# Kernel optimization log

Measured on AMD Instinct MI355X. Metric: run time of the kernel, lower is better.

Reference implementation:

```python
import jax, jax.numpy as jnp
import numpy as np

NUM_HEADS = 12


def setup_inputs() -> dict:
    key = jax.random.key(0)
    ks = jax.random.split(key, 20)
    T, B, D = 1024, 8, 768
    s = 1.0 / np.sqrt(D)
    inp = {
        "query": jax.random.normal(ks[0], (T, B, D), jnp.float32),
        "key": jax.random.normal(ks[1], (T, B, D), jnp.float32),
        "value": jax.random.normal(ks[2], (T, B, D), jnp.float32),
        "ls_len": 512,
    }
    names = ["Wq", "Wk", "Wv", "Wqm", "Wkm", "Wvm", "Wo"]
    for i, n in enumerate(names):
        inp[n] = jax.random.normal(ks[3 + i], (D, D), jnp.float32) * s
        inp["b" + n[1:]] = jnp.zeros((D,), jnp.float32)
    return inp


def reference(query, key, value, ls_len, Wq, bq, Wk, bk, Wv, bv,
              Wqm, bqm, Wkm, bkm, Wvm, bvm, Wo, bo):
    T, B, D = query.shape
    H = NUM_HEADS
    hd = D // H
    scaling = float(hd) ** -0.5

    def proj(x, W, b):
        return x @ W.T + b

    # modal-split projections along the sequence (dim 0), then re-concat
    q = jnp.concatenate([proj(query[:ls_len], Wq, bq),
                         proj(query[ls_len:], Wqm, bqm)], axis=0) * scaling
    k = jnp.concatenate([proj(key[:ls_len], Wk, bk),
                         proj(key[ls_len:], Wkm, bkm)], axis=0)
    v = jnp.concatenate([proj(value[:ls_len], Wv, bv),
                         proj(value[ls_len:], Wvm, bvm)], axis=0)

    # (T, B, D) -> (B*H, T, hd)
    def to_heads(x):
        return x.reshape(x.shape[0], B * H, hd).transpose(1, 0, 2)

    q, k, v = to_heads(q), to_heads(k), to_heads(v)
    scores = jnp.einsum("bth,bsh->bts", q, k)        # (B*H, T, S)
    attn = jax.nn.softmax(scores, axis=-1)
    out = jnp.einsum("bts,bsh->bth", attn, v)        # (B*H, T, hd)
    out = out.transpose(1, 0, 2).reshape(T, B, D)
    return out @ Wo.T + bo
```

## Files before the change

### kernel.cpp

```cpp
#include <hip/hip_runtime.h>

#define T_  1024
#define B_  8
#define D_  768
#define H_  12
#define HD_ 64
#define BH_ 96
#define M_  8192
#define XSZ 6291456ull
#define WSZ 589824ull

typedef __attribute__((ext_vector_type(8))) short short8;
typedef __attribute__((ext_vector_type(4))) float f32x4;

__device__ __forceinline__ unsigned short f2bf(float f) {
    unsigned int u = __float_as_uint(f);
    u += 0x7FFF + ((u >> 16) & 1);
    return (unsigned short)(u >> 16);
}

__device__ __forceinline__ void g2lds16(const unsigned short* g, unsigned short* l) {
    __builtin_amdgcn_global_load_lds(
        (const __attribute__((address_space(1))) unsigned int*)(g),
        (__attribute__((address_space(3))) unsigned int*)(l),
        16, 0, 0);
}

__global__ __launch_bounds__(256)
void convert_kernel(const float* __restrict__ q, const float* __restrict__ k,
                    const float* __restrict__ v,
                    const float* __restrict__ wq, const float* __restrict__ wk,
                    const float* __restrict__ wv, const float* __restrict__ wqm,
                    const float* __restrict__ wkm, const float* __restrict__ wvm,
                    const float* __restrict__ wo,
                    unsigned short* __restrict__ dst)
{
    const int seg = blockIdx.y;
    const float* s; size_t off, n;
    switch (seg) {
        case 0: s = q;   off = 0;               n = XSZ; break;
        case 1: s = k;   off = XSZ;             n = XSZ; break;
        case 2: s = v;   off = 2*XSZ;           n = XSZ; break;
        case 3: s = wq;  off = 3*XSZ;           n = WSZ; break;
        case 4: s = wk;  off = 3*XSZ +   WSZ;   n = WSZ; break;
        case 5: s = wv;  off = 3*XSZ + 2*WSZ;   n = WSZ; break;
        case 6: s = wqm; off = 3*XSZ + 3*WSZ;   n = WSZ; break;
        case 7: s = wkm; off = 3*XSZ + 4*WSZ;   n = WSZ; break;
        case 8: s = wvm; off = 3*XSZ + 5*WSZ;   n = WSZ; break;
        default:s = wo;  off = 3*XSZ + 6*WSZ;   n = WSZ; break;
    }
    unsigned short* d = dst + off;
    const size_t stride = (size_t)gridDim.x * blockDim.x;
    for (size_t i = (size_t)blockIdx.x * blockDim.x + threadIdx.x; i < n / 4; i += stride) {
        const float4 f = reinterpret_cast<const float4*>(s)[i];
        ushort4 o;
        o.x = f2bf(f.x); o.y = f2bf(f.y); o.z = f2bf(f.z); o.w = f2bf(f.w);
        reinterpret_cast<ushort4*>(d)[i] = o;
    }
}

__device__ __forceinline__ void stage_tile64(const unsigned short* __restrict__ A,
                                             const unsigned short* __restrict__ B,
                                             int m0, int n0, int ks,
                                             unsigned short* lds, int buf, int tid)
{
    const int w = tid >> 6, l = tid & 63;
    const int rsub = l >> 3;
    const int csw  = (l & 7) ^ rsub;
    const int koff = ks * 64 + csw * 8;
    #pragma unroll
    for (int p = 0; p < 4; ++p) {
        const int rbase = p * 32 + w * 8;
        const int row   = rbase + rsub;
        g2lds16(&A[(size_t)(m0 + row) * D_ + koff],
                &lds[buf * 16384 + rbase * 64]);
        g2lds16(&B[(size_t)(n0 + row) * D_ + koff],
                &lds[buf * 16384 + 8192 + rbase * 64]);
    }
}

__device__ __forceinline__ void mfma_step64(const unsigned short* lds, int buf,
                                            int wr, int wc, int lr, int lg,
                                            f32x4 acc[4][4])
{
    #pragma unroll
    for (int kk = 0; kk < 2; ++kk) {
        short8 a[4], b[4];
        #pragma unroll
        for (int m = 0; m < 4; ++m) {
            const int row  = wr * 64 + 16 * m + lr;
            const int slot = (kk * 4 + lg) ^ (lr & 7);
            a[m] = *reinterpret_cast<const short8*>(
                &lds[buf * 16384 + row * 64 + slot * 8]);
        }
        #pragma unroll
        for (int n = 0; n < 4; ++n) {
            const int row  = wc * 64 + 16 * n + lr;
            const int slot = (kk * 4 + lg) ^ (lr & 7);
            b[n] = *reinterpret_cast<const short8*>(
                &lds[buf * 16384 + 8192 + row * 64 + slot * 8]);
        }
        #pragma unroll
        for (int m = 0; m < 4; ++m)
            #pragma unroll
            for (int n = 0; n < 4; ++n)
                acc[m][n] = __builtin_amdgcn_mfma_f32_16x16x32_bf16(a[m], b[n], acc[m][n], 0, 0, 0);
    }
}

#define GEMM_CORE(Aptr, Bptr)                                                  \
    f32x4 acc[4][4];                                                           \
    _Pragma("unroll") for (int m = 0; m < 4; ++m)                              \
        _Pragma("unroll") for (int n = 0; n < 4; ++n)                          \
            acc[m][n] = (f32x4){0.f, 0.f, 0.f, 0.f};                           \
    stage_tile64(Aptr, Bptr, m0, n0, 0, lds, 0, tid);                          \
    asm volatile("s_waitcnt vmcnt(0)" ::: "memory");                           \
    __builtin_amdgcn_s_barrier();                                              \
    for (int ks = 0; ks < 12; ++ks) {                                          \
        __builtin_amdgcn_sched_barrier(0);                                     \
        if (ks < 11) stage_tile64(Aptr, Bptr, m0, n0, ks + 1, lds, (ks + 1) & 1, tid); \
        mfma_step64(lds, ks & 1, wr, wc, lr, lg, acc);                         \
        asm volatile("s_waitcnt vmcnt(0) lgkmcnt(0)" ::: "memory");            \
        __builtin_amdgcn_sched_barrier(0);                                     \
        __builtin_amdgcn_s_barrier();                                          \
        __builtin_amdgcn_sched_barrier(0);                                     \
    }

__global__ __launch_bounds__(256)
void qkv_gemm(const unsigned short* __restrict__ xb,
              const unsigned short* __restrict__ wb,
              const int* __restrict__ ls_ptr,
              const float* __restrict__ bq,  const float* __restrict__ bk,
              const float* __restrict__ bv,  const float* __restrict__ bqm,
              const float* __restrict__ bkm, const float* __restrict__ bvm,
              unsigned short* __restrict__ qh, unsigned short* __restrict__ kh,
              unsigned short* __restrict__ vt)
{
    __shared__ unsigned short lds[32768];
    const int bid = blockIdx.x;
    const int L   = (bid & 7) * 144 + (bid >> 3);
    const int z   = L / 384;
    const int rem = L - z * 384;
    const int mi  = rem / 6;
    const int ni  = rem - mi * 6;
    const int m0 = mi * 128, n0 = ni * 128;

    const int tid = threadIdx.x;
    const int w = tid >> 6, l = tid & 63, lr = l & 15, lg = l >> 4;
    const int wr = w >> 1, wc = w & 1;

    const bool modal = (m0 >= ls_ptr[0] * B_);
    const unsigned short* A = xb + (size_t)z * XSZ;
    const unsigned short* W = wb + (size_t)(z + (modal ? 3 : 0)) * WSZ;
    const float* bias = modal ? (z == 0 ? bqm : z == 1 ? bkm : bvm)
                              : (z == 0 ? bq  : z == 1 ? bk  : bv);

    GEMM_CORE(A, W)

    float bn[4];
    #pragma unroll
    for (int n = 0; n < 4; ++n) bn[n] = bias[n0 + wc * 64 + 16 * n + lr];

    if (z < 2) {
        unsigned short* dst = (z == 0) ? qh : kh;
        const float scale = (z == 0) ? 0.18033688011112042f : 1.0f;
        #pragma unroll
        for (int m = 0; m < 4; ++m) {
            const int grb = m0 + wr * 64 + 16 * m + 4 * lg;
            #pragma unroll
            for (int n = 0; n < 4; ++n) {
                const int gc = n0 + wc * 64 + 16 * n + lr;
                const int h = gc >> 6, e = gc & 63;
                #pragma unroll
                for (int j = 0; j < 4; ++j) {
                    const int gr = grb + j, t = gr >> 3, b = gr & 7;
                    dst[((size_t)(b * H_ + h) * T_ + t) * HD_ + e] =
                        f2bf((acc[m][n][j] + bn[n]) * scale);
                }
            }
        }
    } else {
        #pragma unroll
        for (int m = 0; m < 4; ++m) {
            const int grb = m0 + wr * 64 + 16 * m + 4 * lg;
            #pragma unroll
            for (int n = 0; n < 4; ++n) {
                const int gc = n0 + wc * 64 + 16 * n + lr;
                const int h = gc >> 6, e = gc & 63;
                #pragma unroll
                for (int j = 0; j < 4; ++j) {
                    const int gr = grb + j, t = gr >> 3, b = gr & 7;
                    vt[((size_t)(b * H_ + h) * HD_ + e) * T_ + t] =
                        f2bf(acc[m][n][j] + bn[n]);
                }
            }
        }
    }
}

__global__ __launch_bounds__(256)
void out_gemm(const unsigned short* __restrict__ aob,
              const unsigned short* __restrict__ wo,
              const float* __restrict__ bo, float* __restrict__ out)
{
    __shared__ unsigned short lds[32768];
    const int bid = blockIdx.x;
    const int L   = (bid & 7) * 48 + (bid >> 3);
    const int mi  = L / 6, ni = L - mi * 6;
    const int m0 = mi * 128, n0 = ni * 128;

    const int tid = threadIdx.x;
    const int w = tid >> 6, l = tid & 63, lr = l & 15, lg = l >> 4;
    const int wr = w >> 1, wc = w & 1;

    GEMM_CORE(aob, wo)

    float bn[4];
    #pragma unroll
    for (int n = 0; n < 4; ++n) bn[n] = bo[n0 + wc * 64 + 16 * n + lr];

    #pragma unroll
    for (int m = 0; m < 4; ++m) {
        const int grb = m0 + wr * 64 + 16 * m + 4 * lg;
        #pragma unroll
        for (int n = 0; n < 4; ++n) {
            const int gc = n0 + wc * 64 + 16 * n + lr;
            #pragma unroll
            for (int j = 0; j < 4; ++j) {
                const int gr = grb + j;
                out[(size_t)gr * D_ + gc] = acc[m][n][j] + bn[n];
            }
        }
    }
}

__global__ __launch_bounds__(256)
void attn_kernel_bf16(const unsigned short* __restrict__ qh,
                      const unsigned short* __restrict__ kh,
                      const unsigned short* __restrict__ vt,
                      unsigned short* __restrict__ aob)
{
    const int bid = blockIdx.x;
    const int L   = (bid & 7) * 192 + (bid >> 3);
    const int bh  = L >> 4;
    const int qt  = L & 15;

    const int tid = threadIdx.x;
    const int w   = tid >> 6;
    const int l   = tid & 63;
    const int lr  = l & 15;
    const int lg  = l >> 4;

    __shared__ unsigned short Ks[64 * 64];
    __shared__ unsigned short Vt[64 * 64];
    __shared__ unsigned short Ps[64 * 64];

    const size_t qk_head = (size_t)bh * T_ * HD_;
    const size_t vt_head = (size_t)bh * HD_ * T_;

    short8 qf[2];
    #pragma unroll
    for (int c = 0; c < 2; ++c)
        qf[c] = *reinterpret_cast<const short8*>(
            &qh[qk_head + (size_t)(qt * 64 + 16 * w + lr) * HD_ + 8 * lg + 32 * c]);

    const short one_bf = (short)0x3F80;
    const short8 ones8 = {one_bf, one_bf, one_bf, one_bf,
                          one_bf, one_bf, one_bf, one_bf};

    f32x4 o[4];
    #pragma unroll
    for (int ef = 0; ef < 4; ++ef) o[ef] = (f32x4){0.f, 0.f, 0.f, 0.f};
    f32x4 lsumf = (f32x4){0.f, 0.f, 0.f, 0.f};

    for (int kt = 0; kt < 16; ++kt) {
        __syncthreads();
        #pragma unroll
        for (int p = 0; p < 2; ++p) {
            const int slot = tid + p * 256;
            const int row  = slot >> 3;
            const int ch   = slot & 7;
            const int sw   = (ch ^ (row & 7)) * 8;
            const short8 kd = *reinterpret_cast<const short8*>(
                &kh[qk_head + (size_t)(kt * 64 + row) * HD_ + 8 * ch]);
            *reinterpret_cast<short8*>(&Ks[row * 64 + sw]) = kd;
            const short8 vd = *reinterpret_cast<const short8*>(
                &vt[vt_head + (size_t)row * T_ + kt * 64 + 8 * ch]);
            *reinterpret_cast<short8*>(&Vt[row * 64 + sw]) = vd;
        }
        __syncthreads();

        f32x4 s[4];
        #pragma unroll
        for (int nf = 0; nf < 4; ++nf) s[nf] = (f32x4){0.f, 0.f, 0.f, 0.f};
        #pragma unroll
        for (int c = 0; c < 2; ++c) {
            #pragma unroll
            for (int nf = 0; nf < 4; ++nf) {
                const int row = 16 * nf + lr;
                const short8 kb = *reinterpret_cast<const short8*>(
                    &Ks[row * 64 + ((8 * lg + 32 * c) ^ ((row & 7) << 3))]);
                s[nf] = __builtin_amdgcn_mfma_f32_16x16x32_bf16(qf[c], kb, s[nf], 0, 0, 0);
            }
        }

        #pragma unroll
        for (int r = 0; r < 4; ++r) {
            const int q  = 16 * w + 4 * lg + r;
            const int qx = ((4 * lg + r) & 7) << 3;
            #pragma unroll
            for (int nf = 0; nf < 4; ++nf)
                Ps[q * 64 + ((16 * nf + lr) ^ qx)] =
                    f2bf(exp2f(s[nf][r] - 16.0f));
        }
        __syncthreads();

        const int prow = 16 * w + lr;
        #pragma unroll
        for (int c = 0; c < 2; ++c) {
            const short8 pa = *reinterpret_cast<const short8*>(
                &Ps[prow * 64 + ((8 * lg + 32 * c) ^ ((prow & 7) << 3))]);
            #pragma unroll
            for (int ef = 0; ef < 4; ++ef) {
                const int vrow = 16 * ef + lr;
                const short8 vb = *reinterpret_cast<const short8*>(
                    &Vt[vrow * 64 + ((8 * lg + 32 * c) ^ ((vrow & 7) << 3))]);
                o[ef] = __builtin_amdgcn_mfma_f32_16x16x32_bf16(pa, vb, o[ef], 0, 0, 0);
            }
            lsumf = __builtin_amdgcn_mfma_f32_16x16x32_bf16(pa, ones8, lsumf, 0, 0, 0);
        }
    }

    const int b = bh / H_, h = bh % H_;
    #pragma unroll
    for (int r = 0; r < 4; ++r) {
        const int t = qt * 64 + 16 * w + 4 * lg + r;
        const float inv = 1.0f / lsumf[r];
        #pragma unroll
        for (int ef = 0; ef < 4; ++ef)
            aob[((size_t)t * B_ + b) * D_ + h * HD_ + 16 * ef + lr] =
                f2bf(o[ef][r] * inv);
    }
}

extern "C" void kernel_launch(void* const* d_in, const int* in_sizes, int n_in,
                              void* d_out, int out_size, void* d_ws, size_t ws_size,
                              hipStream_t stream)
{
    const float* query = (const float*)d_in[0];
    const float* keyi  = (const float*)d_in[1];
    const float* value = (const float*)d_in[2];
    const int*   lsp   = (const int*)  d_in[3];
    const float* Wq  = (const float*)d_in[4],  *bq  = (const float*)d_in[5];
    const float* Wk  = (const float*)d_in[6],  *bk  = (const float*)d_in[7];
    const float* Wv  = (const float*)d_in[8],  *bv  = (const float*)d_in[9];
    const float* Wqm = (const float*)d_in[10], *bqm = (const float*)d_in[11];
    const float* Wkm = (const float*)d_in[12], *bkm = (const float*)d_in[13];
    const float* Wvm = (const float*)d_in[14], *bvm = (const float*)d_in[15];
    const float* Wo  = (const float*)d_in[16], *bo  = (const float*)d_in[17];

    unsigned short* ws = (unsigned short*)d_ws;
    unsigned short* xb  = ws;
    unsigned short* wb  = xb + 3 * XSZ;
    unsigned short* qh  = wb + 7 * WSZ;
    unsigned short* kh  = qh + XSZ;
    unsigned short* vt  = kh + XSZ;
    unsigned short* aob = vt + XSZ;

    dim3 gc_(512, 10);
    convert_kernel<<<gc_, 256, 0, stream>>>(query, keyi, value,
                                            Wq, Wk, Wv, Wqm, Wkm, Wvm, Wo, xb);

    qkv_gemm<<<1152, 256, 0, stream>>>(xb, wb, lsp, bq, bk, bv, bqm, bkm, bvm,
                                       qh, kh, vt);

    attn_kernel_bf16<<<1536, 256, 0, stream>>>(qh, kh, vt, aob);

    out_gemm<<<384, 256, 0, stream>>>(aob, wb + 6 * WSZ, bo, (float*)d_out);
}
```

Measured before the change: 197.1 us.

## Halve GEMM k-tile, double-buffer attention K/V with async LDS loads, 128-query blocks

The shared GEMM core now stages 32-wide k-slices instead of 64, which halves LDS per block and allows more resident blocks, at the cost of twice as many barriers. The attention kernel moves to 512-thread blocks covering 128 queries, so each K/V tile is reused by twice as many query rows. K/V tiles are now loaded with direct global-to-LDS loads into a double buffer, prefetching the next tile while the current one is computed. This replaces the old register-staged loads and the two syncthreads that had no overlap between loading and compute.

```diff
diff --git a/kernel.cpp b/kernel.cpp
--- a/kernel.cpp
+++ b/kernel.cpp
@@ -59,53 +59,45 @@
     }
 }
 
-__device__ __forceinline__ void stage_tile64(const unsigned short* __restrict__ A,
+__device__ __forceinline__ void stage_tile32(const unsigned short* __restrict__ A,
                                              const unsigned short* __restrict__ B,
                                              int m0, int n0, int ks,
                                              unsigned short* lds, int buf, int tid)
 {
     const int w = tid >> 6, l = tid & 63;
-    const int rsub = l >> 3;
-    const int csw  = (l & 7) ^ rsub;
-    const int koff = ks * 64 + csw * 8;
-    #pragma unroll
-    for (int p = 0; p < 4; ++p) {
-        const int rbase = p * 32 + w * 8;
+    const int rsub = l >> 2;
+    const int cg   = (l & 3) ^ ((l >> 3) & 3);
+    const int koff = ks * 32 + cg * 8;
+    #pragma unroll
+    for (int p = 0; p < 2; ++p) {
+        const int rbase = p * 64 + w * 16;
         const int row   = rbase + rsub;
         g2lds16(&A[(size_t)(m0 + row) * D_ + koff],
-                &lds[buf * 16384 + rbase * 64]);
+                &lds[buf * 8192 + rbase * 32]);
         g2lds16(&B[(size_t)(n0 + row) * D_ + koff],
-                &lds[buf * 16384 + 8192 + rbase * 64]);
-    }
-}
-
-__device__ __forceinline__ void mfma_step64(const unsigned short* lds, int buf,
+                &lds[buf * 8192 + 4096 + rbase * 32]);
+    }
+}
+
+__device__ __forceinline__ void mfma_step32(const unsigned short* lds, int buf,
                                             int wr, int wc, int lr, int lg,
                                             f32x4 acc[4][4])
 {
-    #pragma unroll
-    for (int kk = 0; kk < 2; ++kk) {
-        short8 a[4], b[4];
-        #pragma unroll
-        for (int m = 0; m < 4; ++m) {
-            const int row  = wr * 64 + 16 * m + lr;
-            const int slot = (kk * 4 + lg) ^ (lr & 7);
-            a[m] = *reinterpret_cast<const short8*>(
-                &lds[buf * 16384 + row * 64 + slot * 8]);
-        }
-        #pragma unroll
-        for (int n = 0; n < 4; ++n) {
-            const int row  = wc * 64 + 16 * n + lr;
-            const int slot = (kk * 4 + lg) ^ (lr & 7);
-            b[n] = *reinterpret_cast<const short8*>(
-                &lds[buf * 16384 + 8192 + row * 64 + slot * 8]);
-        }
-        #pragma unroll
-        for (int m = 0; m < 4; ++m)
-            #pragma unroll
-            for (int n = 0; n < 4; ++n)
-                acc[m][n] = __builtin_amdgcn_mfma_f32_16x16x32_bf16(a[m], b[n], acc[m][n], 0, 0, 0);
-    }
+    const int slot = (lg ^ ((lr >> 1) & 3)) * 8;
+    short8 a[4], b[4];
+    #pragma unroll
+    for (int m = 0; m < 4; ++m)
+        a[m] = *reinterpret_cast<const short8*>(
+            &lds[buf * 8192 + (wr * 64 + 16 * m + lr) * 32 + slot]);
+    #pragma unroll
+    for (int n = 0; n < 4; ++n)
+        b[n] = *reinterpret_cast<const short8*>(
+            &lds[buf * 8192 + 4096 + (wc * 64 + 16 * n + lr) * 32 + slot]);
+    #pragma unroll
+    for (int m = 0; m < 4; ++m)
+        #pragma unroll
+        for (int n = 0; n < 4; ++n)
+            acc[m][n] = __builtin_amdgcn_mfma_f32_16x16x32_bf16(a[m], b[n], acc[m][n], 0, 0, 0);
 }
 
 #define GEMM_CORE(Aptr, Bptr)                                                  \
@@ -113,13 +105,13 @@
     _Pragma("unroll") for (int m = 0; m < 4; ++m)                              \
         _Pragma("unroll") for (int n = 0; n < 4; ++n)                          \
             acc[m][n] = (f32x4){0.f, 0.f, 0.f, 0.f};                           \
-    stage_tile64(Aptr, Bptr, m0, n0, 0, lds, 0, tid);                          \
+    stage_tile32(Aptr, Bptr, m0, n0, 0, lds, 0, tid);                          \
     asm volatile("s_waitcnt vmcnt(0)" ::: "memory");                           \
     __builtin_amdgcn_s_barrier();                                              \
-    for (int ks = 0; ks < 12; ++ks) {                                          \
+    for (int ks = 0; ks < 24; ++ks) {                                          \
         __builtin_amdgcn_sched_barrier(0);                                     \
-        if (ks < 11) stage_tile64(Aptr, Bptr, m0, n0, ks + 1, lds, (ks + 1) & 1, tid); \
-        mfma_step64(lds, ks & 1, wr, wc, lr, lg, acc);                         \
+        if (ks < 23) stage_tile32(Aptr, Bptr, m0, n0, ks + 1, lds, (ks + 1) & 1, tid); \
+        mfma_step32(lds, ks & 1, wr, wc, lr, lg, acc);                         \
         asm volatile("s_waitcnt vmcnt(0) lgkmcnt(0)" ::: "memory");            \
         __builtin_amdgcn_sched_barrier(0);                                     \
         __builtin_amdgcn_s_barrier();                                          \
@@ -136,7 +128,7 @@
               unsigned short* __restrict__ qh, unsigned short* __restrict__ kh,
               unsigned short* __restrict__ vt)
 {
-    __shared__ unsigned short lds[32768];
+    __shared__ unsigned short lds[16384];
     const int bid = blockIdx.x;
     const int L   = (bid & 7) * 144 + (bid >> 3);
     const int z   = L / 384;
@@ -203,7 +195,7 @@
               const unsigned short* __restrict__ wo,
               const float* __restrict__ bo, float* __restrict__ out)
 {
-    __shared__ unsigned short lds[32768];
+    __shared__ unsigned short lds[16384];
     const int bid = blockIdx.x;
     const int L   = (bid & 7) * 48 + (bid >> 3);
     const int mi  = L / 6, ni = L - mi * 6;
@@ -234,16 +226,28 @@
     }
 }
 
-__global__ __launch_bounds__(256)
+__device__ __forceinline__ void stage_kv(const unsigned short* __restrict__ khh,
+                                         const unsigned short* __restrict__ vth,
+                                         int kt, unsigned short* KsB,
+                                         unsigned short* VtB, int w, int l)
+{
+    const int rbase = w * 8;
+    const int row   = rbase + (l >> 3);
+    const int cg    = (l & 7) ^ ((l >> 3) & 7);
+    g2lds16(&khh[(size_t)(kt * 64 + row) * HD_ + cg * 8], &KsB[rbase * 64]);
+    g2lds16(&vth[(size_t)row * T_ + kt * 64 + cg * 8],    &VtB[rbase * 64]);
+}
+
+__global__ __launch_bounds__(512)
 void attn_kernel_bf16(const unsigned short* __restrict__ qh,
                       const unsigned short* __restrict__ kh,
                       const unsigned short* __restrict__ vt,
                       unsigned short* __restrict__ aob)
 {
     const int bid = blockIdx.x;
-    const int L   = (bid & 7) * 192 + (bid >> 3);
-    const int bh  = L >> 4;
-    const int qt  = L & 15;
+    const int L   = (bid & 7) * 96 + (bid >> 3);
+    const int bh  = L >> 3;
+    const int qt  = L & 7;
 
     const int tid = threadIdx.x;
     const int w   = tid >> 6;
@@ -251,18 +255,19 @@
     const int lr  = l & 15;
     const int lg  = l >> 4;
 
-    __shared__ unsigned short Ks[64 * 64];
-    __shared__ unsigned short Vt[64 * 64];
-    __shared__ unsigned short Ps[64 * 64];
-
+    __shared__ unsigned short Ks[2][4096];
+    __shared__ unsigned short Vt[2][4096];
+    __shared__ unsigned short Ps[8192];
+
+    const unsigned short* khh = kh + (size_t)bh * T_ * HD_;
+    const unsigned short* vth = vt + (size_t)bh * HD_ * T_;
     const size_t qk_head = (size_t)bh * T_ * HD_;
-    const size_t vt_head = (size_t)bh * HD_ * T_;
 
     short8 qf[2];
     #pragma unroll
     for (int c = 0; c < 2; ++c)
         qf[c] = *reinterpret_cast<const short8*>(
-            &qh[qk_head + (size_t)(qt * 64 + 16 * w + lr) * HD_ + 8 * lg + 32 * c]);
+            &qh[qk_head + (size_t)(qt * 128 + 16 * w + lr) * HD_ + 8 * lg + 32 * c]);
 
     const short one_bf = (short)0x3F80;
     const short8 ones8 = {one_bf, one_bf, one_bf, one_bf,
@@ -273,22 +278,15 @@
     for (int ef = 0; ef < 4; ++ef) o[ef] = (f32x4){0.f, 0.f, 0.f, 0.f};
     f32x4 lsumf = (f32x4){0.f, 0.f, 0.f, 0.f};
 
+    stage_kv(khh, vth, 0, Ks[0], Vt[0], w, l);
+    asm volatile("s_waitcnt vmcnt(0)" ::: "memory");
+    __builtin_amdgcn_s_barrier();
+
+    int buf = 0;
     for (int kt = 0; kt < 16; ++kt) {
-        __syncthreads();
-        #pragma unroll
-        for (int p = 0; p < 2; ++p) {
-            const int slot = tid + p * 256;
-            const int row  = slot >> 3;
-            const int ch   = slot & 7;
-            const int sw   = (ch ^ (row & 7)) * 8;
-            const short8 kd = *reinterpret_cast<const short8*>(
-                &kh[qk_head + (size_t)(kt * 64 + row) * HD_ + 8 * ch]);
-            *reinterpret_cast<short8*>(&Ks[row * 64 + sw]) = kd;
-            const short8 vd = *reinterpret_cast<const short8*>(
-                &vt[vt_head + (size_t)row * T_ + kt * 64 + 8 * ch]);
-            *reinterpret_cast<short8*>(&Vt[row * 64 + sw]) = vd;
-        }
-        __syncthreads();
+        __builtin_amdgcn_sched_barrier(0);
+        if (kt < 15)
+            stage_kv(khh, vth, kt + 1, Ks[buf ^ 1], Vt[buf ^ 1], w, l);
 
         f32x4 s[4];
         #pragma unroll
@@ -297,9 +295,8 @@
         for (int c = 0; c < 2; ++c) {
             #pragma unroll
             for (int nf = 0; nf < 4; ++nf) {
-                const int row = 16 * nf + lr;
                 const short8 kb = *reinterpret_cast<const short8*>(
-                    &Ks[row * 64 + ((8 * lg + 32 * c) ^ ((row & 7) << 3))]);
+                    &Ks[buf][(16 * nf + lr) * 64 + ((8 * lg + 32 * c) ^ ((lr & 7) << 3))]);
                 s[nf] = __builtin_amdgcn_mfma_f32_16x16x32_bf16(qf[c], kb, s[nf], 0, 0, 0);
             }
         }
@@ -313,7 +310,10 @@
                 Ps[q * 64 + ((16 * nf + lr) ^ qx)] =
                     f2bf(exp2f(s[nf][r] - 16.0f));
         }
-        __syncthreads();
+        asm volatile("s_waitcnt lgkmcnt(0)" ::: "memory");
+        __builtin_amdgcn_sched_barrier(0);
+        __builtin_amdgcn_s_barrier();
+        __builtin_amdgcn_sched_barrier(0);
 
         const int prow = 16 * w + lr;
         #pragma unroll
@@ -322,19 +322,24 @@
                 &Ps[prow * 64 + ((8 * lg + 32 * c) ^ ((prow & 7) << 3))]);
             #pragma unroll
             for (int ef = 0; ef < 4; ++ef) {
-                const int vrow = 16 * ef + lr;
                 const short8 vb = *reinterpret_cast<const short8*>(
-                    &Vt[vrow * 64 + ((8 * lg + 32 * c) ^ ((vrow & 7) << 3))]);
+                    &Vt[buf][(16 * ef + lr) * 64 + ((8 * lg + 32 * c) ^ ((lr & 7) << 3))]);
                 o[ef] = __builtin_amdgcn_mfma_f32_16x16x32_bf16(pa, vb, o[ef], 0, 0, 0);
             }
             lsumf = __builtin_amdgcn_mfma_f32_16x16x32_bf16(pa, ones8, lsumf, 0, 0, 0);
         }
+
+        asm volatile("s_waitcnt vmcnt(0) lgkmcnt(0)" ::: "memory");
+        __builtin_amdgcn_sched_barrier(0);
+        __builtin_amdgcn_s_barrier();
+        __builtin_amdgcn_sched_barrier(0);
+        buf ^= 1;
     }
 
     const int b = bh / H_, h = bh % H_;
     #pragma unroll
     for (int r = 0; r < 4; ++r) {
-        const int t = qt * 64 + 16 * w + 4 * lg + r;
+        const int t = qt * 128 + 16 * w + 4 * lg + r;
         const float inv = 1.0f / lsumf[r];
         #pragma unroll
         for (int ef = 0; ef < 4; ++ef)
@@ -374,7 +379,7 @@
     qkv_gemm<<<1152, 256, 0, stream>>>(xb, wb, lsp, bq, bk, bv, bqm, bkm, bvm,
                                        qh, kh, vt);
 
-    attn_kernel_bf16<<<1536, 256, 0, stream>>>(qh, kh, vt, aob);
+    attn_kernel_bf16<<<768, 512, 0, stream>>>(qh, kh, vt, aob);
 
     out_gemm<<<384, 256, 0, stream>>>(aob, wb + 6 * WSZ, bo, (float*)d_out);
 }
```

New measurement: 187.4 us. -4.9%, faster.
